# Performance work log

Measured on AMD Instinct MI355X. Metric: run time of the kernel, lower is better.

The kernel has to match this reference:

```python
import jax, jax.numpy as jnp
import numpy as np

N_NODES = 100000
N_EDGES = 1600000
IN_F = 512
OUT_F = 256
ORDER = 2


def setup_inputs() -> dict:
    key = jax.random.key(0)
    k1, k2, k3, k4, k5 = jax.random.split(key, 5)
    features = jax.random.normal(k1, (N_NODES, IN_F), dtype=jnp.float32)
    # Xavier-uniform init like torch.nn.init.xavier_uniform_
    limit = float(np.sqrt(6.0 / (IN_F + OUT_F)))
    weight = jax.random.uniform(k2, (IN_F, OUT_F), dtype=jnp.float32, minval=-limit, maxval=limit)
    row = jnp.sort(jax.random.randint(k3, (N_EDGES,), 0, N_NODES, dtype=jnp.int32))
    col = jax.random.randint(k4, (N_EDGES,), 0, N_NODES, dtype=jnp.int32)
    adj_vals = jax.random.uniform(k5, (N_EDGES,), dtype=jnp.float32)
    return {"features": features, "weight": weight, "row": row, "col": col, "adj_vals": adj_vals}


def _spmm(row, col, vals, x, n):
    # out[i] = sum_{e: row[e]==i} vals[e] * x[col[e]]  (COO sparse @ dense)
    msgs = vals[:, None] * x[col]  # [E, F]
    return jax.ops.segment_sum(msgs, row, num_segments=n)


def reference(features, weight, row, col, adj_vals):
    out = jnp.tanh(features @ weight)  # dense mm + tanh (active=True)
    for _ in range(ORDER):  # spmm once, then order-1 more times
        out = _spmm(row, col, adj_vals, out, N_NODES)
    return out
```

## Files before the change

kernel.cpp:

```cpp
#include <hip/hip_runtime.h>
#include <hip/hip_bf16.h>

#define M_NODES 100000
#define N_EDGES 1600000
#define K_IN 512
#define N_OUT 256

typedef short bf16x8 __attribute__((ext_vector_type(8)));
typedef float f32x4 __attribute__((ext_vector_type(4)));

__device__ inline unsigned short f2bf_u(float f) {
  union { float f; unsigned u; } x; x.f = f;
  unsigned r = x.u + 0x7FFFu + ((x.u >> 16) & 1u);
  return (unsigned short)(r >> 16);
}
__device__ inline float bfu2f(unsigned short h) {
  union { unsigned u; float f; } x; x.u = ((unsigned)h) << 16;
  return x.f;
}
__device__ inline float fast_tanh(float x) {
  float ax = __builtin_fabsf(x);
  float z = __expf(-2.0f * ax);
  float t = (1.0f - z) * __builtin_amdgcn_rcpf(1.0f + z);
  return __builtin_copysignf(t, x);
}

__global__ void prep_w_kernel(const float* __restrict__ w, short* __restrict__ wt) {
  int idx = blockIdx.x * 256 + threadIdx.x;
  int k = idx >> 8, n = idx & 255;
  wt[n * K_IN + k] = (short)f2bf_u(w[idx]);
}

__global__ void build_rp_kernel(const int* __restrict__ row, int* __restrict__ rp) {
  int r = blockIdx.x * 256 + threadIdx.x;
  if (r > M_NODES) return;
  int lo = 0, hi = N_EDGES;
  while (lo < hi) {
    int mid = (lo + hi) >> 1;
    if (row[mid] < r) lo = mid + 1; else hi = mid;
  }
  rp[r] = lo;
}

__global__ __launch_bounds__(256, 2) void gemm_tanh_kernel(
    const float* __restrict__ A, const short* __restrict__ Wt,
    unsigned short* __restrict__ H) {
  const int tid = threadIdx.x;
  const int wave = tid >> 6, lane = tid & 63;
  const int quad = lane >> 4, l16 = lane & 15;
  const int R0 = (blockIdx.x * 4 + wave) * 32;

  f32x4 acc[2][16];
  #pragma unroll
  for (int m = 0; m < 2; ++m)
    #pragma unroll
    for (int n = 0; n < 16; ++n) acc[m][n] = (f32x4){0.f, 0.f, 0.f, 0.f};

  const float* Ab0;
  const float* Ab1;
  {
    int g0 = min(R0 + l16, M_NODES - 1);
    int g1 = min(R0 + 16 + l16, M_NODES - 1);
    Ab0 = A + (size_t)g0 * K_IN + quad * 8;
    Ab1 = A + (size_t)g1 * K_IN + quad * 8;
  }
  const short* Bb = Wt + (size_t)l16 * K_IN + quad * 8;

  float4 a00 = *(const float4*)(Ab0);
  float4 a01 = *(const float4*)(Ab0 + 4);
  float4 a10 = *(const float4*)(Ab1);
  float4 a11 = *(const float4*)(Ab1 + 4);

  for (int ks = 0; ks < 16; ++ks) {
    bf16x8 af0, af1;
    {
      union { unsigned short s[8]; bf16x8 v; } u;
      u.s[0]=f2bf_u(a00.x); u.s[1]=f2bf_u(a00.y); u.s[2]=f2bf_u(a00.z); u.s[3]=f2bf_u(a00.w);
      u.s[4]=f2bf_u(a01.x); u.s[5]=f2bf_u(a01.y); u.s[6]=f2bf_u(a01.z); u.s[7]=f2bf_u(a01.w);
      af0 = u.v;
      u.s[0]=f2bf_u(a10.x); u.s[1]=f2bf_u(a10.y); u.s[2]=f2bf_u(a10.z); u.s[3]=f2bf_u(a10.w);
      u.s[4]=f2bf_u(a11.x); u.s[5]=f2bf_u(a11.y); u.s[6]=f2bf_u(a11.z); u.s[7]=f2bf_u(a11.w);
      af1 = u.v;
    }
    if (ks < 15) {
      const float* p0 = Ab0 + (ks + 1) * 32;
      const float* p1 = Ab1 + (ks + 1) * 32;
      a00 = *(const float4*)(p0);
      a01 = *(const float4*)(p0 + 4);
      a10 = *(const float4*)(p1);
      a11 = *(const float4*)(p1 + 4);
    }
    const short* Bk = Bb + ks * 32;
    #pragma unroll
    for (int nt = 0; nt < 16; ++nt) {
      bf16x8 bfr = *(const bf16x8*)(Bk + (size_t)nt * 16 * K_IN);
      acc[0][nt] = __builtin_amdgcn_mfma_f32_16x16x32_bf16(af0, bfr, acc[0][nt], 0, 0, 0);
      acc[1][nt] = __builtin_amdgcn_mfma_f32_16x16x32_bf16(af1, bfr, acc[1][nt], 0, 0, 0);
    }
  }

  #pragma unroll
  for (int m = 0; m < 2; ++m) {
    #pragma unroll
    for (int rr = 0; rr < 4; ++rr) {
      int row = R0 + m * 16 + quad * 4 + rr;
      if (row < M_NODES) {
        #pragma unroll
        for (int nt = 0; nt < 16; ++nt) {
          H[(size_t)row * N_OUT + nt * 16 + l16] =
              f2bf_u(fast_tanh(acc[m][nt][rr]));
        }
      }
    }
  }
}

__global__ __launch_bounds__(256) void spmm_bf_bf(
    const int* __restrict__ rp, const int* __restrict__ colv,
    const float* __restrict__ vals, const unsigned short* __restrict__ x,
    unsigned short* __restrict__ y) {
  int w = (blockIdx.x * 256 + threadIdx.x) >> 6;
  int lane = threadIdx.x & 63;
  int i = __builtin_amdgcn_readfirstlane(w);
  int s = rp[i], e = rp[i + 1];
  float a0 = 0.f, a1 = 0.f, a2 = 0.f, a3 = 0.f;
  const unsigned short* xl = x + lane * 4;
  for (int base = s; base < e; base += 64) {
    int nn = min(e - base, 64);
    int tl = min(base + lane, e - 1);
    int c_l = colv[tl];
    float v_l = vals[tl];
    int tt = 0;
    for (; tt + 8 <= nn; tt += 8) {
      ushort4 xv[8]; float vv[8];
      #pragma unroll
      for (int j = 0; j < 8; ++j) {
        int c = __shfl(c_l, tt + j);
        vv[j] = __shfl(v_l, tt + j);
        xv[j] = *(const ushort4*)(xl + (size_t)c * N_OUT);
      }
      #pragma unroll
      for (int j = 0; j < 8; ++j) {
        a0 += vv[j] * bfu2f(xv[j].x); a1 += vv[j] * bfu2f(xv[j].y);
        a2 += vv[j] * bfu2f(xv[j].z); a3 += vv[j] * bfu2f(xv[j].w);
      }
    }
    for (; tt + 4 <= nn; tt += 4) {
      ushort4 xv[4]; float vv[4];
      #pragma unroll
      for (int j = 0; j < 4; ++j) {
        int c = __shfl(c_l, tt + j);
        vv[j] = __shfl(v_l, tt + j);
        xv[j] = *(const ushort4*)(xl + (size_t)c * N_OUT);
      }
      #pragma unroll
      for (int j = 0; j < 4; ++j) {
        a0 += vv[j] * bfu2f(xv[j].x); a1 += vv[j] * bfu2f(xv[j].y);
        a2 += vv[j] * bfu2f(xv[j].z); a3 += vv[j] * bfu2f(xv[j].w);
      }
    }
    for (; tt < nn; ++tt) {
      int c = __shfl(c_l, tt);
      float v = __shfl(v_l, tt);
      ushort4 xv = *(const ushort4*)(xl + (size_t)c * N_OUT);
      a0 += v * bfu2f(xv.x); a1 += v * bfu2f(xv.y);
      a2 += v * bfu2f(xv.z); a3 += v * bfu2f(xv.w);
    }
  }
  ushort4 o;
  o.x = f2bf_u(a0); o.y = f2bf_u(a1); o.z = f2bf_u(a2); o.w = f2bf_u(a3);
  *(ushort4*)(y + (size_t)i * N_OUT + lane * 4) = o;
}

__global__ __launch_bounds__(256) void spmm_bf_f32(
    const int* __restrict__ rp, const int* __restrict__ colv,
    const float* __restrict__ vals, const unsigned short* __restrict__ x,
    float* __restrict__ y) {
  int w = (blockIdx.x * 256 + threadIdx.x) >> 6;
  int lane = threadIdx.x & 63;
  int i = __builtin_amdgcn_readfirstlane(w);
  int s = rp[i], e = rp[i + 1];
  float a0 = 0.f, a1 = 0.f, a2 = 0.f, a3 = 0.f;
  const unsigned short* xl = x + lane * 4;
  for (int base = s; base < e; base += 64) {
    int nn = min(e - base, 64);
    int tl = min(base + lane, e - 1);
    int c_l = colv[tl];
    float v_l = vals[tl];
    int tt = 0;
    for (; tt + 8 <= nn; tt += 8) {
      ushort4 xv[8]; float vv[8];
      #pragma unroll
      for (int j = 0; j < 8; ++j) {
        int c = __shfl(c_l, tt + j);
        vv[j] = __shfl(v_l, tt + j);
        xv[j] = *(const ushort4*)(xl + (size_t)c * N_OUT);
      }
      #pragma unroll
      for (int j = 0; j < 8; ++j) {
        a0 += vv[j] * bfu2f(xv[j].x); a1 += vv[j] * bfu2f(xv[j].y);
        a2 += vv[j] * bfu2f(xv[j].z); a3 += vv[j] * bfu2f(xv[j].w);
      }
    }
    for (; tt + 4 <= nn; tt += 4) {
      ushort4 xv[4]; float vv[4];
      #pragma unroll
      for (int j = 0; j < 4; ++j) {
        int c = __shfl(c_l, tt + j);
        vv[j] = __shfl(v_l, tt + j);
        xv[j] = *(const ushort4*)(xl + (size_t)c * N_OUT);
      }
      #pragma unroll
      for (int j = 0; j < 4; ++j) {
        a0 += vv[j] * bfu2f(xv[j].x); a1 += vv[j] * bfu2f(xv[j].y);
        a2 += vv[j] * bfu2f(xv[j].z); a3 += vv[j] * bfu2f(xv[j].w);
      }
    }
    for (; tt < nn; ++tt) {
      int c = __shfl(c_l, tt);
      float v = __shfl(v_l, tt);
      ushort4 xv = *(const ushort4*)(xl + (size_t)c * N_OUT);
      a0 += v * bfu2f(xv.x); a1 += v * bfu2f(xv.y);
      a2 += v * bfu2f(xv.z); a3 += v * bfu2f(xv.w);
    }
  }
  float4 o = {a0, a1, a2, a3};
  *(float4*)(y + (size_t)i * N_OUT + lane * 4) = o;
}

extern "C" void kernel_launch(void* const* d_in, const int* in_sizes, int n_in,
                              void* d_out, int out_size, void* d_ws, size_t ws_size,
                              hipStream_t stream) {
  const float* features = (const float*)d_in[0];
  const float* weight   = (const float*)d_in[1];
  const int*   row      = (const int*)d_in[2];
  const int*   col      = (const int*)d_in[3];
  const float* vals     = (const float*)d_in[4];
  float* out = (float*)d_out;

  char* ws = (char*)d_ws;
  const size_t HB = (size_t)M_NODES * N_OUT * 2;
  const size_t RPB = 400016;
  unsigned short* H  = (unsigned short*)ws;
  unsigned short* y1 = (unsigned short*)(ws + HB);
  int*   rp = (int*)(ws + 2 * HB);
  short* Wt = (short*)(ws + 2 * HB + RPB);

  prep_w_kernel<<<512, 256, 0, stream>>>(weight, Wt);
  build_rp_kernel<<<(M_NODES + 1 + 255) / 256, 256, 0, stream>>>(row, rp);
  gemm_tanh_kernel<<<(M_NODES + 127) / 128, 256, 0, stream>>>(features, Wt, H);
  spmm_bf_bf<<<25000, 256, 0, stream>>>(rp, col, vals, H, y1);
  spmm_bf_f32<<<25000, 256, 0, stream>>>(rp, col, vals, y1, out);
}
```

Before: 649.5 us.

## Pre-swizzle weights into MFMA fragments and software-pipeline GEMM loads

The weight prep kernel now writes bf16 weights in MFMA-fragment order, so each lane reads a contiguous 16-byte fragment. The GEMM becomes one wave per 32-row block, with double-buffered A and B register fragments prefetched around sched barriers, and f32-to-bf16 conversion now uses the packed v_cvt_pk_bf16_f32 instruction. The row bounds checks are dropped because 100000 rows split exactly into 3125 blocks. Register pressure rises from holding prefetched B fragments, and the packed convert may round differently from the manual round-to-nearest-even code.

```diff
diff --git a/kernel.cpp b/kernel.cpp
--- a/kernel.cpp
+++ b/kernel.cpp
@@ -24,11 +24,26 @@
   float t = (1.0f - z) * __builtin_amdgcn_rcpf(1.0f + z);
   return __builtin_copysignf(t, x);
 }
+__device__ inline bf16x8 cvt8(float4 lo, float4 hi) {
+  union { unsigned u[4]; bf16x8 v; } r;
+  asm("v_cvt_pk_bf16_f32 %0, %1, %2" : "=v"(r.u[0]) : "v"(lo.x), "v"(lo.y));
+  asm("v_cvt_pk_bf16_f32 %0, %1, %2" : "=v"(r.u[1]) : "v"(lo.z), "v"(lo.w));
+  asm("v_cvt_pk_bf16_f32 %0, %1, %2" : "=v"(r.u[2]) : "v"(hi.x), "v"(hi.y));
+  asm("v_cvt_pk_bf16_f32 %0, %1, %2" : "=v"(r.u[3]) : "v"(hi.z), "v"(hi.w));
+  return r.v;
+}
 
 __global__ void prep_w_kernel(const float* __restrict__ w, short* __restrict__ wt) {
-  int idx = blockIdx.x * 256 + threadIdx.x;
-  int k = idx >> 8, n = idx & 255;
-  wt[n * K_IN + k] = (short)f2bf_u(w[idx]);
+  int frag = blockIdx.x * 256 + threadIdx.x;
+  int lane = frag & 63;
+  int fi = frag >> 6;
+  int ks = fi >> 4, nt = fi & 15;
+  int quad = lane >> 4, l16 = lane & 15;
+  int n = nt * 16 + l16;
+  int k0 = ks * 32 + quad * 8;
+  #pragma unroll
+  for (int j = 0; j < 8; ++j)
+    wt[(size_t)frag * 8 + j] = (short)f2bf_u(w[(size_t)(k0 + j) * N_OUT + n]);
 }
 
 __global__ void build_rp_kernel(const int* __restrict__ row, int* __restrict__ rp) {
@@ -42,75 +57,98 @@
   rp[r] = lo;
 }
 
-__global__ __launch_bounds__(256, 2) void gemm_tanh_kernel(
-    const float* __restrict__ A, const short* __restrict__ Wt,
+__global__ __launch_bounds__(64, 2) void gemm_tanh_kernel(
+    const float* __restrict__ A, const short* __restrict__ WtF,
     unsigned short* __restrict__ H) {
-  const int tid = threadIdx.x;
-  const int wave = tid >> 6, lane = tid & 63;
+  const int lane = threadIdx.x;
   const int quad = lane >> 4, l16 = lane & 15;
-  const int R0 = (blockIdx.x * 4 + wave) * 32;
-
-  f32x4 acc[2][16];
-  #pragma unroll
-  for (int m = 0; m < 2; ++m)
-    #pragma unroll
-    for (int n = 0; n < 16; ++n) acc[m][n] = (f32x4){0.f, 0.f, 0.f, 0.f};
-
-  const float* Ab0;
-  const float* Ab1;
-  {
-    int g0 = min(R0 + l16, M_NODES - 1);
-    int g1 = min(R0 + 16 + l16, M_NODES - 1);
-    Ab0 = A + (size_t)g0 * K_IN + quad * 8;
-    Ab1 = A + (size_t)g1 * K_IN + quad * 8;
-  }
-  const short* Bb = Wt + (size_t)l16 * K_IN + quad * 8;
-
-  float4 a00 = *(const float4*)(Ab0);
-  float4 a01 = *(const float4*)(Ab0 + 4);
-  float4 a10 = *(const float4*)(Ab1);
-  float4 a11 = *(const float4*)(Ab1 + 4);
-
-  for (int ks = 0; ks < 16; ++ks) {
-    bf16x8 af0, af1;
-    {
-      union { unsigned short s[8]; bf16x8 v; } u;
-      u.s[0]=f2bf_u(a00.x); u.s[1]=f2bf_u(a00.y); u.s[2]=f2bf_u(a00.z); u.s[3]=f2bf_u(a00.w);
-      u.s[4]=f2bf_u(a01.x); u.s[5]=f2bf_u(a01.y); u.s[6]=f2bf_u(a01.z); u.s[7]=f2bf_u(a01.w);
-      af0 = u.v;
-      u.s[0]=f2bf_u(a10.x); u.s[1]=f2bf_u(a10.y); u.s[2]=f2bf_u(a10.z); u.s[3]=f2bf_u(a10.w);
-      u.s[4]=f2bf_u(a11.x); u.s[5]=f2bf_u(a11.y); u.s[6]=f2bf_u(a11.z); u.s[7]=f2bf_u(a11.w);
-      af1 = u.v;
-    }
-    if (ks < 15) {
-      const float* p0 = Ab0 + (ks + 1) * 32;
-      const float* p1 = Ab1 + (ks + 1) * 32;
-      a00 = *(const float4*)(p0);
-      a01 = *(const float4*)(p0 + 4);
-      a10 = *(const float4*)(p1);
-      a11 = *(const float4*)(p1 + 4);
-    }
-    const short* Bk = Bb + ks * 32;
-    #pragma unroll
-    for (int nt = 0; nt < 16; ++nt) {
-      bf16x8 bfr = *(const bf16x8*)(Bk + (size_t)nt * 16 * K_IN);
-      acc[0][nt] = __builtin_amdgcn_mfma_f32_16x16x32_bf16(af0, bfr, acc[0][nt], 0, 0, 0);
-      acc[1][nt] = __builtin_amdgcn_mfma_f32_16x16x32_bf16(af1, bfr, acc[1][nt], 0, 0, 0);
-    }
-  }
-
-  #pragma unroll
-  for (int m = 0; m < 2; ++m) {
+  const int R0 = blockIdx.x * 32;
+
+  f32x4 acc0[16], acc1[16];
+  #pragma unroll
+  for (int i = 0; i < 16; ++i) {
+    acc0[i] = (f32x4){0.f, 0.f, 0.f, 0.f};
+    acc1[i] = (f32x4){0.f, 0.f, 0.f, 0.f};
+  }
+
+  const float* Ab0 = A + (size_t)(R0 + l16) * K_IN + quad * 8;
+  const float* Ab1 = Ab0 + (size_t)16 * K_IN;
+  const short* Bb = WtF + lane * 8;
+
+  float4 aA[4], aB[4];
+  bf16x8 bP[8], bQ[8];
+
+  aA[0] = *(const float4*)(Ab0);      aA[1] = *(const float4*)(Ab0 + 4);
+  aA[2] = *(const float4*)(Ab1);      aA[3] = *(const float4*)(Ab1 + 4);
+  aB[0] = *(const float4*)(Ab0 + 32); aB[1] = *(const float4*)(Ab0 + 36);
+  aB[2] = *(const float4*)(Ab1 + 32); aB[3] = *(const float4*)(Ab1 + 36);
+  #pragma unroll
+  for (int nt = 0; nt < 8; ++nt)
+    bP[nt] = *(const bf16x8*)(Bb + (size_t)nt * 512);
+  #pragma unroll
+  for (int nt = 0; nt < 8; ++nt)
+    bQ[nt] = *(const bf16x8*)(Bb + (size_t)(8 + nt) * 512);
+
+  #pragma unroll
+  for (int p = 0; p < 8; ++p) {
+    const int ks1 = 2 * p + 1;
+    bf16x8 af0 = cvt8(aA[0], aA[1]);
+    bf16x8 af1 = cvt8(aA[2], aA[3]);
+    #pragma unroll
+    for (int nt = 0; nt < 8; ++nt) {
+      acc0[nt] = __builtin_amdgcn_mfma_f32_16x16x32_bf16(af0, bP[nt], acc0[nt], 0, 0, 0);
+      acc1[nt] = __builtin_amdgcn_mfma_f32_16x16x32_bf16(af1, bP[nt], acc1[nt], 0, 0, 0);
+    }
+    #pragma unroll
+    for (int nt = 0; nt < 8; ++nt)
+      bP[nt] = *(const bf16x8*)(Bb + (size_t)(ks1 * 16 + nt) * 512);
+    #pragma unroll
+    for (int nt = 0; nt < 8; ++nt) {
+      acc0[8 + nt] = __builtin_amdgcn_mfma_f32_16x16x32_bf16(af0, bQ[nt], acc0[8 + nt], 0, 0, 0);
+      acc1[8 + nt] = __builtin_amdgcn_mfma_f32_16x16x32_bf16(af1, bQ[nt], acc1[8 + nt], 0, 0, 0);
+    }
+    #pragma unroll
+    for (int nt = 0; nt < 8; ++nt)
+      bQ[nt] = *(const bf16x8*)(Bb + (size_t)(ks1 * 16 + 8 + nt) * 512);
+    bf16x8 ag0 = cvt8(aB[0], aB[1]);
+    bf16x8 ag1 = cvt8(aB[2], aB[3]);
+    if (p < 7) {
+      __builtin_amdgcn_sched_barrier(0);
+      const float* pa0 = Ab0 + (2 * p + 2) * 32;
+      const float* pa1 = Ab1 + (2 * p + 2) * 32;
+      aA[0] = *(const float4*)(pa0);      aA[1] = *(const float4*)(pa0 + 4);
+      aA[2] = *(const float4*)(pa1);      aA[3] = *(const float4*)(pa1 + 4);
+      aB[0] = *(const float4*)(pa0 + 32); aB[1] = *(const float4*)(pa0 + 36);
+      aB[2] = *(const float4*)(pa1 + 32); aB[3] = *(const float4*)(pa1 + 36);
+      __builtin_amdgcn_sched_barrier(0);
+    }
+    #pragma unroll
+    for (int nt = 0; nt < 8; ++nt) {
+      acc0[nt] = __builtin_amdgcn_mfma_f32_16x16x32_bf16(ag0, bP[nt], acc0[nt], 0, 0, 0);
+      acc1[nt] = __builtin_amdgcn_mfma_f32_16x16x32_bf16(ag1, bP[nt], acc1[nt], 0, 0, 0);
+    }
+    #pragma unroll
+    for (int nt = 0; nt < 8; ++nt) {
+      acc0[8 + nt] = __builtin_amdgcn_mfma_f32_16x16x32_bf16(ag0, bQ[nt], acc0[8 + nt], 0, 0, 0);
+      acc1[8 + nt] = __builtin_amdgcn_mfma_f32_16x16x32_bf16(ag1, bQ[nt], acc1[8 + nt], 0, 0, 0);
+    }
+    if (p < 7) {
+      #pragma unroll
+      for (int nt = 0; nt < 8; ++nt)
+        bP[nt] = *(const bf16x8*)(Bb + (size_t)((ks1 + 1) * 16 + nt) * 512);
+      #pragma unroll
+      for (int nt = 0; nt < 8; ++nt)
+        bQ[nt] = *(const bf16x8*)(Bb + (size_t)((ks1 + 1) * 16 + 8 + nt) * 512);
+    }
+  }
+
+  #pragma unroll
+  for (int nt = 0; nt < 16; ++nt) {
     #pragma unroll
     for (int rr = 0; rr < 4; ++rr) {
-      int row = R0 + m * 16 + quad * 4 + rr;
-      if (row < M_NODES) {
-        #pragma unroll
-        for (int nt = 0; nt < 16; ++nt) {
-          H[(size_t)row * N_OUT + nt * 16 + l16] =
-              f2bf_u(fast_tanh(acc[m][nt][rr]));
-        }
-      }
+      int r0 = R0 + quad * 4 + rr;
+      H[(size_t)r0 * N_OUT + nt * 16 + l16] = f2bf_u(fast_tanh(acc0[nt][rr]));
+      H[(size_t)(r0 + 16) * N_OUT + nt * 16 + l16] = f2bf_u(fast_tanh(acc1[nt][rr]));
     }
   }
 }
@@ -246,9 +284,9 @@
   int*   rp = (int*)(ws + 2 * HB);
   short* Wt = (short*)(ws + 2 * HB + RPB);
 
-  prep_w_kernel<<<512, 256, 0, stream>>>(weight, Wt);
+  prep_w_kernel<<<64, 256, 0, stream>>>(weight, Wt);
   build_rp_kernel<<<(M_NODES + 1 + 255) / 256, 256, 0, stream>>>(row, rp);
-  gemm_tanh_kernel<<<(M_NODES + 127) / 128, 256, 0, stream>>>(features, Wt, H);
+  gemm_tanh_kernel<<<3125, 64, 0, stream>>>(features, Wt, H);
   spmm_bf_bf<<<25000, 256, 0, stream>>>(rp, col, vals, H, y1);
   spmm_bf_f32<<<25000, 256, 0, stream>>>(rp, col, vals, y1, out);
 }
```

New measurement: 592.9 us. 1.1x faster.
